# Performance work log

Measured on AMD Instinct MI355X. Metric: run time of the kernel, lower is better.

## Reference

```python
import jax, jax.numpy as jnp
import numpy as np

D = 128
H = 4
DK = D // H


def _spmm(row, col, val, x, n):
    # sparse.mm(adj, x) with adj in COO form: out[row] += val * x[col]
    return jax.ops.segment_sum(val[:, None] * x[col], row, num_segments=n)


def _arrg(h, a1_w, a1_b, a2_w, a2_b):
    return jax.nn.leaky_relu(h @ a1_w + a1_b, negative_slope=0.01) @ a2_w + a2_b


def _cross_attn(x, q_x, q_w, k_w, v_w):
    n, d = x.shape
    m = q_x.shape[0]
    q = (q_x @ q_w).reshape(m, H, DK).transpose(1, 0, 2)   # [H, Q, dk]
    k = (x @ k_w).reshape(n, H, DK).transpose(1, 0, 2)     # [H, N, dk]
    v = (q_x @ v_w).reshape(m, H, DK).transpose(1, 0, 2)   # [H, Q, dk]
    s = jnp.einsum('hnd,hqd->hnq', k, q) / jnp.sqrt(jnp.float32(DK))
    w = jax.nn.softmax(s, axis=-1)                          # softmax over queries
    out = jnp.einsum('hnq,hqd->hnd', w, v).transpose(1, 0, 2).reshape(n, d)
    return out + x


def setup_inputs() -> dict:
    key = jax.random.key(0)
    ks = iter(jax.random.split(key, 64))
    nrm = lambda shape, s=0.05: jax.random.normal(next(ks), shape, jnp.float32) * s
    inp = {}
    inp['trans_w'] = nrm((1, D)); inp['trans_b'] = nrm((D,))
    inp['g_w'] = nrm((D, D));     inp['g_b'] = nrm((D,))
    inp['qg_w'] = nrm((D, D));    inp['qg_b'] = nrm((D,))
    inp['q_w'] = nrm((D, D)); inp['k_w'] = nrm((D, D)); inp['v_w'] = nrm((D, D))
    inp['a1_w'] = nrm((D, 2 * D)); inp['a1_b'] = nrm((2 * D,))
    inp['a2_w'] = nrm((2 * D, D)); inp['a2_b'] = nrm((D,))
    inp['x0'] = jax.random.normal(next(ks), (25000,), jnp.float32)
    inp['q0'] = jax.random.normal(next(ks), (100,), jnp.float32)
    for i in (1, 2, 3):
        inp[f'xin{i}'] = jax.random.normal(next(ks), (25000,), jnp.float32)
        inp[f'qin{i}'] = jax.random.normal(next(ks), (100,), jnp.float32)
    n_sizes = {1: 50000, 2: 75000, 3: 100000}
    q_sizes = {1: 200, 2: 300, 3: 400}
    for i in (1, 2, 3):
        e = 16 * n_sizes[i]
        inp[f'aval{i}'] = jax.random.uniform(next(ks), (e,), jnp.float32)
        inp[f'arow{i}'] = jax.random.randint(next(ks), (e,), 0, n_sizes[i], jnp.int64)
        inp[f'acol{i}'] = jax.random.randint(next(ks), (e,), 0, n_sizes[i], jnp.int64)
        qe = 16 * q_sizes[i]
        inp[f'qval{i}'] = jax.random.uniform(next(ks), (qe,), jnp.float32)
        inp[f'qrow{i}'] = jax.random.randint(next(ks), (qe,), 0, q_sizes[i], jnp.int64)
        inp[f'qcol{i}'] = jax.random.randint(next(ks), (qe,), 0, q_sizes[i], jnp.int64)
    return inp


def reference(trans_w, trans_b, g_w, g_b, qg_w, qg_b, q_w, k_w, v_w,
              a1_w, a1_b, a2_w, a2_b,
              x0, q0, xin1, xin2, xin3, qin1, qin2, qin3,
              aval1, aval2, aval3, qval1, qval2, qval3,
              arow1, acol1, arow2, acol2, arow3, acol3,
              qrow1, qcol1, qrow2, qcol2, qrow3, qcol3):
    trans = lambda v: v[:, None] @ trans_w + trans_b
    x = trans(x0)
    qx = trans(q0)
    steps = [
        (xin1, qin1, arow1, acol1, aval1, qrow1, qcol1, qval1, 50000, 200),
        (xin2, qin2, arow2, acol2, aval2, qrow2, qcol2, qval2, 75000, 300),
        (xin3, qin3, arow3, acol3, aval3, qrow3, qcol3, qval3, 100000, 400),
    ]
    for xin, qin, ar, ac, av, qr, qc, qv, n, m in steps:
        x = jnp.concatenate([x, trans(xin)], axis=0)
        qx = jnp.concatenate([qx, trans(qin)], axis=0)
        x = _spmm(ar, ac, av, x @ g_w + g_b, n)
        qx = _spmm(qr, qc, qv, qx @ qg_w + qg_b, m)
        x = _arrg(x, a1_w, a1_b, a2_w, a2_b)
        qx = _arrg(qx, a1_w, a1_b, a2_w, a2_b)
        x = _cross_attn(x, qx, q_w, k_w, v_w)
    return (x, qx)
```

## Files before the change

### kernel.cpp

```cpp
#include <hip/hip_runtime.h>

typedef unsigned short u16;
typedef __attribute__((ext_vector_type(8))) short bf16x8;
typedef __attribute__((ext_vector_type(4))) float f32x4;
typedef __attribute__((ext_vector_type(2))) unsigned u32x2;

__device__ __forceinline__ float b2f(u16 v) {
    return __uint_as_float(((unsigned)v) << 16);
}
__device__ __forceinline__ u16 f2b(float x) {
    unsigned u = __float_as_uint(x);
    unsigned r = u + 0x7FFFu + ((u >> 16) & 1u);
    return (u16)(r >> 16);
}
__device__ __forceinline__ float4 load_bf4(const u16* p) {
    ushort4 q = *(const ushort4*)p;
    float4 f;
    f.x = b2f(q.x); f.y = b2f(q.y); f.z = b2f(q.z); f.w = b2f(q.w);
    return f;
}
__device__ __forceinline__ float4 in4(const void* p, long off, bool bf) {
    if (bf) return load_bf4((const u16*)p + off);
    return *(const float4*)((const float*)p + off);
}
__device__ __forceinline__ float in1(const void* p, long off, bool bf) {
    if (bf) return b2f(((const u16*)p)[off]);
    return ((const float*)p)[off];
}
__device__ __forceinline__ int inIdx(const void* p, long i, bool i64) {
    return ((const int*)p)[i64 ? 2 * i : i];
}

__global__ void sniff_kernel(const u16* __restrict__ x0bits, const int* __restrict__ arow,
                             int* __restrict__ flags) {
    if (threadIdx.x != 0 || blockIdx.x != 0) return;
    int plaus = 0;
    for (int i = 0; i < 256; ++i) {
        u16 v = x0bits[i];
        int e = (v >> 7) & 0xFF;
        if (v == 0 || (e >= 100 && e <= 135)) plaus++;
    }
    flags[0] = (plaus >= 200) ? 1 : 0;
    int nz = 0;
    for (int i = 1; i < 128; i += 2) nz += (arow[i] != 0);
    flags[1] = (nz == 0) ? 1 : 0;
}

__global__ void trans2_kernel(const void* __restrict__ vx, float* __restrict__ outx, int rowsx,
                              const void* __restrict__ vq, float* __restrict__ outq, int rowsq,
                              const void* __restrict__ tw, const void* __restrict__ tb,
                              const int* __restrict__ flags) {
    const bool bf = flags[0] != 0;
    int t = blockIdx.x * blockDim.x + threadIdx.x;
    int c4 = (t & 31) * 4;
    int r = t >> 5;
    const void* v; float* out;
    if (r < rowsx) { v = vx; out = outx; }
    else { r -= rowsx; if (r >= rowsq) return; v = vq; out = outq; }
    float vv = in1(v, r, bf);
    float4 w4 = in4(tw, c4, bf);
    float4 b4 = in4(tb, c4, bf);
    float4 o;
    o.x = vv * w4.x + b4.x; o.y = vv * w4.y + b4.y;
    o.z = vv * w4.z + b4.z; o.w = vv * w4.w + b4.w;
    *(float4*)(out + (size_t)r * 128 + c4) = o;
}

__global__ void wprep_all_kernel(const void* __restrict__ g_w, const void* __restrict__ qg_w,
                                 const void* __restrict__ a1_w, const void* __restrict__ a2_w,
                                 const void* __restrict__ k_w, const void* __restrict__ q_w,
                                 const void* __restrict__ v_w,
                                 u16* __restrict__ Wg, u16* __restrict__ Wqg,
                                 u16* __restrict__ Wa1, u16* __restrict__ Wa2,
                                 u16* __restrict__ Wk, u16* __restrict__ Wq,
                                 u16* __restrict__ Wv, const int* __restrict__ flags) {
    const bool bf = flags[0] != 0;
    int idx = blockIdx.x * blockDim.x + threadIdx.x;
    const void* src; u16* dst; int K, N, loc;
    if (idx < 32768) {
        if (idx < 16384) { src = g_w; dst = Wg; loc = idx; }
        else { src = qg_w; dst = Wqg; loc = idx - 16384; }
        K = 128; N = 128;
    } else if (idx < 65536) { src = a1_w; dst = Wa1; loc = idx - 32768; K = 128; N = 256; }
    else if (idx < 98304)  { src = a2_w; dst = Wa2; loc = idx - 65536; K = 256; N = 128; }
    else if (idx < 147456) {
        if (idx < 114688) { src = k_w; dst = Wk; loc = idx - 98304; }
        else if (idx < 131072) { src = q_w; dst = Wq; loc = idx - 114688; }
        else { src = v_w; dst = Wv; loc = idx - 131072; }
        K = 128; N = 128;
    } else return;
    int j = loc & 7, lane = (loc >> 3) & 63, t = loc >> 9;
    int KC = K >> 5;
    int kc = t % KC, ct = t / KC;
    int k = kc * 32 + (lane >> 4) * 8 + j;
    int nn = ct * 16 + (lane & 15);
    dst[loc] = f2b(in1(src, (long)k * N + nn, bf));
}

template<int KTOT, int NOUT, bool LEAKY, typename AT, typename CT>
__launch_bounds__(256)
__global__ void gemm_mfma_kernel(const AT* __restrict__ A, const u16* __restrict__ Wf,
                                 const void* __restrict__ bias, CT* __restrict__ C,
                                 int n, const int* __restrict__ flags,
                                 const void* __restrict__ vap, int nprevP,
                                 const void* __restrict__ twp, const void* __restrict__ tbp) {
    constexpr int KC = KTOT / 32;
    constexpr int NT = NOUT / 16;
    __shared__ u16 wlds[KTOT * NOUT];
    {
        const int4* srcw = (const int4*)Wf;
        int4* dstw = (int4*)wlds;
        constexpr int NV = KTOT * NOUT * 2 / 16;
#pragma unroll
        for (int i = 0; i < NV / 256; ++i)
            dstw[i * 256 + threadIdx.x] = srcw[i * 256 + threadIdx.x];
    }
    __syncthreads();
    const bool bf = flags[0] != 0;
    const int lane = threadIdx.x & 63;
    const int wave = threadIdx.x >> 6;
    const int quad = lane >> 4, col = lane & 15;
    const int rbase = (blockIdx.x * 4 + wave) * 16;
    if (rbase >= n) return;
    int node = rbase + col; if (node >= n) node = n - 1;
    f32x4 acc[NT];
#pragma unroll
    for (int ct = 0; ct < NT; ++ct) acc[ct] = (f32x4){0.f, 0.f, 0.f, 0.f};
#pragma unroll
    for (int kc = 0; kc < KC; ++kc) {
        bf16x8 af;
        if constexpr (sizeof(AT) == 2) {
            af = *(const bf16x8*)((const u16*)A + (size_t)node * KTOT + kc * 32 + quad * 8);
        } else {
            int c0 = kc * 32 + quad * 8;
            if (vap && node >= nprevP) {
                float v = in1(vap, node - nprevP, bf);
                float4 w0 = in4(twp, c0, bf), w1 = in4(twp, c0 + 4, bf);
                float4 b0 = in4(tbp, c0, bf), b1 = in4(tbp, c0 + 4, bf);
                af[0] = (short)f2b(v * w0.x + b0.x); af[1] = (short)f2b(v * w0.y + b0.y);
                af[2] = (short)f2b(v * w0.z + b0.z); af[3] = (short)f2b(v * w0.w + b0.w);
                af[4] = (short)f2b(v * w1.x + b1.x); af[5] = (short)f2b(v * w1.y + b1.y);
                af[6] = (short)f2b(v * w1.z + b1.z); af[7] = (short)f2b(v * w1.w + b1.w);
            } else {
                const float* ap = (const float*)A + (size_t)node * KTOT + c0;
                float4 a0 = *(const float4*)ap;
                float4 a1 = *(const float4*)(ap + 4);
                af[0] = (short)f2b(a0.x); af[1] = (short)f2b(a0.y);
                af[2] = (short)f2b(a0.z); af[3] = (short)f2b(a0.w);
                af[4] = (short)f2b(a1.x); af[5] = (short)f2b(a1.y);
                af[6] = (short)f2b(a1.z); af[7] = (short)f2b(a1.w);
            }
        }
#pragma unroll
        for (int ct = 0; ct < NT; ++ct) {
            bf16x8 wf = *(const bf16x8*)(wlds + (((ct * KC + kc) * 64 + lane) * 8));
            acc[ct] = __builtin_amdgcn_mfma_f32_16x16x32_bf16(af, wf, acc[ct], 0, 0, 0);
        }
    }
#pragma unroll
    for (int ct = 0; ct < NT; ++ct) {
        int colg = ct * 16 + col;
        float b = bias ? in1(bias, colg, bf) : 0.f;
#pragma unroll
        for (int r = 0; r < 4; ++r) {
            int row = rbase + quad * 4 + r;
            if (row >= n) continue;
            float v = acc[ct][r] + b;
            if (LEAKY) v = v > 0.f ? v : 0.01f * v;
            if constexpr (sizeof(CT) == 2) C[(size_t)row * NOUT + colg] = (CT)f2b(v);
            else                           C[(size_t)row * NOUT + colg] = (CT)v;
        }
    }
}

__launch_bounds__(256)
__global__ void gemm_qv_kernel(const float* __restrict__ A, const u16* __restrict__ Wfq,
                               const u16* __restrict__ Wfv, u16* __restrict__ Qf,
                               u16* __restrict__ Vf, int m, int mt32) {
    __shared__ u16 wldsq[128 * 128];
    __shared__ u16 wldsv[128 * 128];
    {
        const int4* sq = (const int4*)Wfq;
        const int4* sv = (const int4*)Wfv;
        int4* dq = (int4*)wldsq;
        int4* dv = (int4*)wldsv;
#pragma unroll
        for (int i = 0; i < 8; ++i) {
            dq[i * 256 + threadIdx.x] = sq[i * 256 + threadIdx.x];
            dv[i * 256 + threadIdx.x] = sv[i * 256 + threadIdx.x];
        }
    }
    __syncthreads();
    const int mpad = mt32 * 32;
    const int mt16 = mt32 * 2;
    const int lane = threadIdx.x & 63;
    const int wave = threadIdx.x >> 6;
    const int quad = lane >> 4, col = lane & 15;
    const int rbase = (blockIdx.x * 4 + wave) * 16;
    if (rbase >= mpad) return;
    int node = rbase + col; if (node >= m) node = m - 1;
    f32x4 accq[8], accv[8];
#pragma unroll
    for (int ct = 0; ct < 8; ++ct) {
        accq[ct] = (f32x4){0.f, 0.f, 0.f, 0.f};
        accv[ct] = (f32x4){0.f, 0.f, 0.f, 0.f};
    }
#pragma unroll
    for (int kc = 0; kc < 4; ++kc) {
        const float* ap = A + (size_t)node * 128 + kc * 32 + quad * 8;
        float4 a0 = *(const float4*)ap;
        float4 a1 = *(const float4*)(ap + 4);
        bf16x8 af;
        af[0] = (short)f2b(a0.x); af[1] = (short)f2b(a0.y);
        af[2] = (short)f2b(a0.z); af[3] = (short)f2b(a0.w);
        af[4] = (short)f2b(a1.x); af[5] = (short)f2b(a1.y);
        af[6] = (short)f2b(a1.z); af[7] = (short)f2b(a1.w);
#pragma unroll
        for (int ct = 0; ct < 8; ++ct) {
            bf16x8 wq = *(const bf16x8*)(wldsq + (((ct * 4 + kc) * 64 + lane) * 8));
            bf16x8 wv = *(const bf16x8*)(wldsv + (((ct * 4 + kc) * 64 + lane) * 8));
            accq[ct] = __builtin_amdgcn_mfma_f32_16x16x32_bf16(af, wq, accq[ct], 0, 0, 0);
            accv[ct] = __builtin_amdgcn_mfma_f32_16x16x32_bf16(af, wv, accv[ct], 0, 0, 0);
        }
    }
    const float qscale = 0.17677669529663687f * 1.44269504088896340736f;
#pragma unroll
    for (int ct = 0; ct < 8; ++ct) {
        int colg = ct * 16 + col;
        int h = colg >> 5, dim = colg & 31;
#pragma unroll
        for (int r = 0; r < 4; ++r) {
            int row = rbase + quad * 4 + r;
            if (row >= mpad) continue;
            bool pad = row >= m;
            float vq = pad ? 0.f : accq[ct][r] * qscale;
            float vv = pad ? 0.f : accv[ct][r];
            {
                size_t idx = ((((size_t)h * mt16 + (row >> 4)) * 64)
                              + ((dim >> 3) << 4) + (row & 15)) * 8 + (dim & 7);
                Qf[idx] = f2b(vq);
            }
            {
                size_t idx = (((((size_t)h * mt32 + (row >> 5)) * 2 + (dim >> 4)) * 64)
                              + (((row >> 3) & 3) << 4) + (dim & 15)) * 8 + (row & 7);
                Vf[idx] = f2b(vv);
            }
        }
    }
}

#define RSH 8
#define NBC_MAX 512
#define EPB 4096
#define BSTRIDE 6144

__global__ void ginit_kernel(int* __restrict__ p, int nbc) {
    int i = blockIdx.x * blockDim.x + threadIdx.x;
    if (i < nbc) p[i] = i * BSTRIDE;
}

__launch_bounds__(256)
__global__ void qbuild_kernel(const void* __restrict__ rows, const void* __restrict__ colsin,
                              const void* __restrict__ valsin, int e, int nrows,
                              int2* __restrict__ pack1, int* __restrict__ rowptr,
                              int* __restrict__ rowend, const int* __restrict__ flags) {
    __shared__ int hist[512], cur[512], sc[512];
    const bool bf = flags[0] != 0;
    const bool i64 = flags[1] != 0;
    const int tid = threadIdx.x;
    for (int i = tid; i < 512; i += 256) hist[i] = 0;
    __syncthreads();
    for (int i = tid; i < e; i += 256)
        atomicAdd(&hist[inIdx(rows, i, i64)], 1);
    __syncthreads();
    int v0 = hist[tid], v1 = hist[tid + 256];
    sc[tid] = v0; sc[tid + 256] = v1;
    __syncthreads();
    for (int off = 1; off < 512; off <<= 1) {
        int a = (tid >= off) ? sc[tid - off] : 0;
        int b = sc[tid + 256 - off];
        __syncthreads();
        sc[tid] += a;
        sc[tid + 256] += b;
        __syncthreads();
    }
    {
        int x = sc[tid] - v0;
        cur[tid] = x;
        if (tid < nrows) { rowptr[tid] = x; rowend[tid] = x + v0; }
        int x1 = sc[tid + 256] - v1;
        cur[tid + 256] = x1;
        if (tid + 256 < nrows) { rowptr[tid + 256] = x1; rowend[tid + 256] = x1 + v1; }
    }
    __syncthreads();
    for (int i = tid; i < e; i += 256) {
        int r = inIdx(rows, i, i64);
        int p = atomicAdd(&cur[r], 1);
        pack1[p] = (int2){inIdx(colsin, i, i64), __float_as_int(in1(valsin, i, bf))};
    }
}

__launch_bounds__(256)
__global__ void psort_kernel(const void* __restrict__ rows, const void* __restrict__ colsin,
                             const void* __restrict__ valsin, int e,
                             int* __restrict__ gcur, int2* __restrict__ pack0,
                             int nbc, const int* __restrict__ flags) {
    __shared__ int hist[NBC_MAX];
    __shared__ int scan[NBC_MAX];
    __shared__ int base[NBC_MAX];
    __shared__ int cur[NBC_MAX];
    __shared__ int2 stage[EPB];
    __shared__ u16 binof[EPB];
    const bool bf = flags[0] != 0;
    const bool i64 = flags[1] != 0;
    const int tid = threadIdx.x;
    const long s0 = (long)blockIdx.x * EPB;
    int cnt_e = e - (int)s0; if (cnt_e > EPB) cnt_e = EPB;

    for (int i = tid; i < NBC_MAX; i += 256) hist[i] = 0;
    __syncthreads();
    for (int j = tid; j < cnt_e; j += 256)
        atomicAdd(&hist[inIdx(rows, s0 + j, i64) >> RSH], 1);
    __syncthreads();
    for (int i = tid; i < NBC_MAX; i += 256) scan[i] = hist[i];
    __syncthreads();
    for (int off = 1; off < NBC_MAX; off <<= 1) {
        int a = (tid >= off) ? scan[tid - off] : 0;
        int c = scan[tid + 256 - off];
        __syncthreads();
        scan[tid] += a;
        scan[tid + 256] += c;
        __syncthreads();
    }
    for (int i = tid; i < nbc; i += 256) {
        int h = hist[i];
        cur[i] = scan[i] - h;
        base[i] = h ? atomicAdd(&gcur[i], h) : 0;
    }
    __syncthreads();
    for (int j = tid; j < cnt_e; j += 256) {
        int r = inIdx(rows, s0 + j, i64);
        int bin = r >> RSH;
        int p = atomicAdd(&cur[bin], 1);
        int2 pk;
        pk.x = ((r & ((1 << RSH) - 1)) << 20) | inIdx(colsin, s0 + j, i64);
        pk.y = __float_as_int(in1(valsin, s0 + j, bf));
        stage[p] = pk;
        binof[p] = (u16)bin;
    }
    __syncthreads();
    for (int j = tid; j < cnt_e; j += 256) {
        int bin = binof[j];
        int st = scan[bin] - hist[bin];
        pack0[base[bin] + (j - st)] = stage[j];
    }
}

__launch_bounds__(256)
__global__ void breorder256_kernel(const int2* __restrict__ pack0, int* __restrict__ bend,
                                   int2* __restrict__ pack1,
                                   int* __restrict__ rowptr, int* __restrict__ rowend, int n) {
    __shared__ int hist[256], scan[256], cur[256];
    const int b = blockIdx.x;
    const int s = b * BSTRIDE, e = bend[b];
    const int tid = threadIdx.x;
    hist[tid] = 0;
    __syncthreads();
    if (tid == 0) bend[b] = b * BSTRIDE;
    for (int i = s + tid; i < e; i += 256)
        atomicAdd(&hist[(unsigned)pack0[i].x >> 20], 1);
    __syncthreads();
    scan[tid] = hist[tid];
    __syncthreads();
    for (int off = 1; off < 256; off <<= 1) {
        int a = (tid >= off) ? scan[tid - off] : 0;
        __syncthreads();
        scan[tid] += a;
        __syncthreads();
    }
    int st = s + scan[tid] - hist[tid];
    cur[tid] = st;
    int rg = (b << RSH) + tid;
    if (rg < n) { rowptr[rg] = st; rowend[rg] = st + hist[tid]; }
    __syncthreads();
    for (int i = s + tid; i < e; i += 256) {
        int2 pk = pack0[i];
        int rl = (unsigned)pk.x >> 20;
        int p = atomicAdd(&cur[rl], 1);
        pack1[p] = (int2){pk.x & 0xFFFFF, pk.y};
    }
}

__device__ __forceinline__ void bffma8(float v, uint4 h, float* a) {
    a[0] += v * __uint_as_float(h.x << 16);
    a[1] += v * __uint_as_float(h.x & 0xFFFF0000u);
    a[2] += v * __uint_as_float(h.y << 16);
    a[3] += v * __uint_as_float(h.y & 0xFFFF0000u);
    a[4] += v * __uint_as_float(h.z << 16);
    a[5] += v * __uint_as_float(h.z & 0xFFFF0000u);
    a[6] += v * __uint_as_float(h.w << 16);
    a[7] += v * __uint_as_float(h.w & 0xFFFF0000u);
}
__global__ void spmm_kernel(const u16* __restrict__ H, const int* __restrict__ rowptr,
                            const int* __restrict__ rowend, const int2* __restrict__ pack,
                            u16* __restrict__ out, int n) {
    int w = threadIdx.x >> 6;
    int lane = threadIdx.x & 63;
    int r = blockIdx.x * 4 + w;
    if (r >= n) return;
    const int s16 = lane >> 4;
    const int l16 = lane & 15;
    int s = rowptr[r], e = rowend[r];
    float a[8] = {0.f, 0.f, 0.f, 0.f, 0.f, 0.f, 0.f, 0.f};
    int i = s + s16;
    for (; i + 12 < e; i += 16) {
        int2 p0 = pack[i], p1 = pack[i + 4], p2 = pack[i + 8], p3 = pack[i + 12];
        uint4 h0 = *(const uint4*)(H + (size_t)p0.x * 128 + l16 * 8);
        uint4 h1 = *(const uint4*)(H + (size_t)p1.x * 128 + l16 * 8);
        uint4 h2 = *(const uint4*)(H + (size_t)p2.x * 128 + l16 * 8);
        uint4 h3 = *(const uint4*)(H + (size_t)p3.x * 128 + l16 * 8);
        bffma8(__int_as_float(p0.y), h0, a);
        bffma8(__int_as_float(p1.y), h1, a);
        bffma8(__int_as_float(p2.y), h2, a);
        bffma8(__int_as_float(p3.y), h3, a);
    }
    for (; i < e; i += 4) {
        int2 p0 = pack[i];
        uint4 h0 = *(const uint4*)(H + (size_t)p0.x * 128 + l16 * 8);
        bffma8(__int_as_float(p0.y), h0, a);
    }
#pragma unroll
    for (int k = 0; k < 8; ++k) {
        a[k] += __shfl_xor(a[k], 16, 64);
        a[k] += __shfl_xor(a[k], 32, 64);
    }
    if (s16 == 0) {
        uint4 o;
        o.x = (unsigned)f2b(a[0]) | ((unsigned)f2b(a[1]) << 16);
        o.y = (unsigned)f2b(a[2]) | ((unsigned)f2b(a[3]) << 16);
        o.z = (unsigned)f2b(a[4]) | ((unsigned)f2b(a[5]) << 16);
        o.w = (unsigned)f2b(a[6]) | ((unsigned)f2b(a[7]) << 16);
        *(uint4*)(out + (size_t)r * 128 + l16 * 8) = o;
    }
}

__launch_bounds__(256)
__global__ void attn_mfma_kernel(const u16* __restrict__ Kb, const u16* __restrict__ Qf,
                                 const u16* __restrict__ Vf, float* __restrict__ X,
                                 int n, int m, int mt32, int pad) {
    __shared__ __align__(128) u16 Pbuf_all[4 * 1024];
    const int h = blockIdx.y;
    const int wave = threadIdx.x >> 6;
    const int lane = threadIdx.x & 63;
    const int nb = (blockIdx.x * 4 + wave) * 32;
    if (nb >= n) return;
    const int quad = lane >> 4, col = lane & 15;
    int node0 = nb + col;      if (node0 >= n) node0 = n - 1;
    int node1 = nb + 16 + col; if (node1 >= n) node1 = n - 1;
    bf16x8 kf0 = *(const bf16x8*)(Kb + (size_t)node0 * 128 + h * 32 + quad * 8);
    bf16x8 kf1 = *(const bf16x8*)(Kb + (size_t)node1 * 128 + h * 32 + quad * 8);
    f32x4 O00 = {0.f, 0.f, 0.f, 0.f}, O01 = {0.f, 0.f, 0.f, 0.f};
    f32x4 O10 = {0.f, 0.f, 0.f, 0.f}, O11 = {0.f, 0.f, 0.f, 0.f};
    const f32x4 zero = {0.f, 0.f, 0.f, 0.f};
    float Lp0[4] = {0.f, 0.f, 0.f, 0.f};
    float Lp1[4] = {0.f, 0.f, 0.f, 0.f};
    u16* Pw0 = Pbuf_all + wave * 1024;
    u16* Pw1 = Pw0 + 512;
    uint2* pw0[2]; uint2* pw1[2];
    pw0[0] = (uint2*)(Pw0 + col * 16 + quad * 4);
    pw0[1] = (uint2*)(Pw0 + 256 + col * 16 + quad * 4);
    pw1[0] = (uint2*)(Pw1 + col * 16 + quad * 4);
    pw1[1] = (uint2*)(Pw1 + 256 + col * 16 + quad * 4);
    const unsigned paddr0 = (unsigned)(uintptr_t)Pw0 + (unsigned)(quad * 256 + col * 8);
    const unsigned paddr1 = (unsigned)(uintptr_t)Pw1 + (unsigned)(quad * 256 + col * 8);
    const u16* Qbase = Qf + (size_t)h * (mt32 * 2) * 512;
    const u16* Vbase = Vf + (size_t)h * mt32 * 1024;
    for (int qc = 0; qc < mt32; ++qc) {
#pragma unroll
        for (int half = 0; half < 2; ++half) {
            bf16x8 qfr = *(const bf16x8*)(Qbase + (size_t)(qc * 2 + half) * 512 + lane * 8);
            f32x4 S0 = __builtin_amdgcn_mfma_f32_16x16x32_bf16(kf0, qfr, zero, 0, 0, 0);
            f32x4 S1 = __builtin_amdgcn_mfma_f32_16x16x32_bf16(kf1, qfr, zero, 0, 0, 0);
            float a0 = __builtin_amdgcn_exp2f(fminf(S0[0], 115.f));
            float a1 = __builtin_amdgcn_exp2f(fminf(S0[1], 115.f));
            float a2 = __builtin_amdgcn_exp2f(fminf(S0[2], 115.f));
            float a3 = __builtin_amdgcn_exp2f(fminf(S0[3], 115.f));
            float b0 = __builtin_amdgcn_exp2f(fminf(S1[0], 115.f));
            float b1 = __builtin_amdgcn_exp2f(fminf(S1[1], 115.f));
            float b2 = __builtin_amdgcn_exp2f(fminf(S1[2], 115.f));
            float b3 = __builtin_amdgcn_exp2f(fminf(S1[3], 115.f));
            Lp0[0] += a0; Lp0[1] += a1; Lp0[2] += a2; Lp0[3] += a3;
            Lp1[0] += b0; Lp1[1] += b1; Lp1[2] += b2; Lp1[3] += b3;
            unsigned ra, rb, rc, rd;
            asm volatile("v_cvt_pk_bf16_f32 %0, %1, %2" : "=v"(ra) : "v"(a0), "v"(a1));
            asm volatile("v_cvt_pk_bf16_f32 %0, %1, %2" : "=v"(rb) : "v"(a2), "v"(a3));
            asm volatile("v_cvt_pk_bf16_f32 %0, %1, %2" : "=v"(rc) : "v"(b0), "v"(b1));
            asm volatile("v_cvt_pk_bf16_f32 %0, %1, %2" : "=v"(rd) : "v"(b2), "v"(b3));
            uint2 pka; pka.x = ra; pka.y = rb;
            uint2 pkb; pkb.x = rc; pkb.y = rd;
            *pw0[half] = pka;
            *pw1[half] = pkb;
        }
        asm volatile("s_waitcnt lgkmcnt(0)" ::: "memory");
        u32x2 t0a, t0b, t1a, t1b;
        asm volatile("ds_read_b64_tr_b16 %0, %1" : "=&v"(t0a) : "v"(paddr0) : "memory");
        asm volatile("ds_read_b64_tr_b16 %0, %1 offset:128" : "=&v"(t0b) : "v"(paddr0) : "memory");
        asm volatile("ds_read_b64_tr_b16 %0, %1" : "=&v"(t1a) : "v"(paddr1) : "memory");
        asm volatile("ds_read_b64_tr_b16 %0, %1 offset:128" : "=&v"(t1b) : "v"(paddr1) : "memory");
        asm volatile("s_waitcnt lgkmcnt(0)" ::: "memory");
        __builtin_amdgcn_sched_barrier(0);
        bf16x8 pf0, pf1;
        ((u32x2*)&pf0)[0] = t0a; ((u32x2*)&pf0)[1] = t0b;
        ((u32x2*)&pf1)[0] = t1a; ((u32x2*)&pf1)[1] = t1b;
        bf16x8 v0 = *(const bf16x8*)(Vbase + (size_t)(qc * 2 + 0) * 512 + lane * 8);
        bf16x8 v1 = *(const bf16x8*)(Vbase + (size_t)(qc * 2 + 1) * 512 + lane * 8);
        __builtin_amdgcn_s_setprio(1);
        O00 = __builtin_amdgcn_mfma_f32_16x16x32_bf16(pf0, v0, O00, 0, 0, 0);
        O01 = __builtin_amdgcn_mfma_f32_16x16x32_bf16(pf0, v1, O01, 0, 0, 0);
        O10 = __builtin_amdgcn_mfma_f32_16x16x32_bf16(pf1, v0, O10, 0, 0, 0);
        O11 = __builtin_amdgcn_mfma_f32_16x16x32_bf16(pf1, v1, O11, 0, 0, 0);
        __builtin_amdgcn_s_setprio(0);
    }
#pragma unroll
    for (int mask = 1; mask < 16; mask <<= 1) {
#pragma unroll
        for (int r = 0; r < 4; ++r) {
            Lp0[r] += __shfl_xor(Lp0[r], mask, 64);
            Lp1[r] += __shfl_xor(Lp1[r], mask, 64);
        }
    }
#pragma unroll
    for (int r = 0; r < 4; ++r) {
        int nd = nb + quad * 4 + r;
        if (nd < n) {
            float inv = 1.f / fmaxf(Lp0[r] - (float)pad, 1e-35f);
            float* xp = X + (size_t)nd * 128 + h * 32;
            xp[col]      += O00[r] * inv;
            xp[16 + col] += O01[r] * inv;
        }
        int nd1 = nb + 16 + quad * 4 + r;
        if (nd1 < n) {
            float inv = 1.f / fmaxf(Lp1[r] - (float)pad, 1e-35f);
            float* xp = X + (size_t)nd1 * 128 + h * 32;
            xp[col]      += O10[r] * inv;
            xp[16 + col] += O11[r] * inv;
        }
    }
}

__global__ void out_writer_kernel(const float* __restrict__ X, const float* __restrict__ QX,
                                  void* __restrict__ out, const int* __restrict__ flags) {
    const bool bf = flags[0] != 0;
    const int n4x = 100000 * 128 / 4;
    const int n4t = n4x + 400 * 128 / 4;
    int i = blockIdx.x * blockDim.x + threadIdx.x;
    if (i >= n4t) return;
    float4 v = (i < n4x) ? ((const float4*)X)[i] : ((const float4*)QX)[i - n4x];
    if (bf) {
        ushort4 q; q.x = f2b(v.x); q.y = f2b(v.y); q.z = f2b(v.z); q.w = f2b(v.w);
        ((ushort4*)out)[i] = q;
    } else {
        ((float4*)out)[i] = v;
    }
}

extern "C" void kernel_launch(void* const* d_in, const int* in_sizes, int n_in,
                              void* d_out, int out_size, void* d_ws, size_t ws_size,
                              hipStream_t stream) {
    (void)n_in; (void)out_size; (void)ws_size;
    const void* trans_w = d_in[0];
    const void* trans_b = d_in[1];
    const void* g_w  = d_in[2];
    const void* g_b  = d_in[3];
    const void* qg_w = d_in[4];
    const void* qg_b = d_in[5];
    const void* q_w  = d_in[6];
    const void* k_w  = d_in[7];
    const void* v_w  = d_in[8];
    const void* a1_w = d_in[9];
    const void* a1_b = d_in[10];
    const void* a2_w = d_in[11];
    const void* a2_b = d_in[12];
    const void* x0   = d_in[13];
    const void* q0   = d_in[14];

    int ixin[3], iqin[3], iaval[3], iarow[3], iacol[3], iqval[3], iqrow[3], iqcol[3];
    if (in_sizes[16] == 100) {
        for (int s = 0; s < 3; ++s) {
            ixin[s] = 15 + 2 * s; iqin[s] = 16 + 2 * s;
            int b = 21 + 6 * s;
            iaval[s] = b; iarow[s] = b + 1; iacol[s] = b + 2;
            iqval[s] = b + 3; iqrow[s] = b + 4; iqcol[s] = b + 5;
        }
    } else {
        int xs[3] = {15,16,17}, qs_[3] = {18,19,20};
        int av[3] = {21,22,23}, qv[3] = {24,25,26};
        int ar[3] = {27,29,31}, ac[3] = {28,30,32};
        int qr[3] = {33,35,37}, qc[3] = {34,36,38};
        for (int s = 0; s < 3; ++s) {
            ixin[s]=xs[s]; iqin[s]=qs_[s]; iaval[s]=av[s]; iqval[s]=qv[s];
            iarow[s]=ar[s]; iacol[s]=ac[s]; iqrow[s]=qr[s]; iqcol[s]=qc[s];
        }
    }

    char* p = (char*)d_ws;
    auto alloc = [&](size_t bytes) -> char* {
        char* r = p;
        p += (bytes + 255) & ~(size_t)255;
        return r;
    };
    int*   flags = (int*)alloc(256);
    const int NMAX = 100000;
    const int NBINS = (NMAX + 255) >> RSH;
    float* X   = (float*)alloc((size_t)NMAX * 128 * 4);
    u16*   T1b = (u16*)  alloc((size_t)NMAX * 128 * 2);
    u16*   Xs  = (u16*)  alloc((size_t)NMAX * 128 * 2);
    u16*   T2  = (u16*)  alloc((size_t)NMAX * 256 * 2);
    float* QX  = (float*)alloc((size_t)400 * 128 * 4);
    u16*   QT1b= (u16*)  alloc((size_t)400 * 128 * 2);
    u16*   QXs = (u16*)  alloc((size_t)400 * 128 * 2);
    u16*   QT2 = (u16*)  alloc((size_t)400 * 256 * 2);
    u16*   Qfrag = (u16*)alloc((size_t)4 * 13 * 1024 * 2);
    u16*   Vfrag = (u16*)alloc((size_t)4 * 13 * 1024 * 2);
    u16* Wg  = (u16*)alloc((size_t)128 * 128 * 2);
    u16* Wqg = (u16*)alloc((size_t)128 * 128 * 2);
    u16* Wa1 = (u16*)alloc((size_t)128 * 256 * 2);
    u16* Wa2 = (u16*)alloc((size_t)256 * 128 * 2);
    u16* Wk  = (u16*)alloc((size_t)128 * 128 * 2);
    u16* Wq  = (u16*)alloc((size_t)128 * 128 * 2);
    u16* Wv  = (u16*)alloc((size_t)128 * 128 * 2);
    int2*  csr_pack = (int2*)alloc((size_t)(NBINS + 1) * BSTRIDE * 8);
    int*   bktcur = (int*)alloc((size_t)NBC_MAX * 4);
    int*   rowptr = (int*)alloc((size_t)NMAX * 4);
    int*   rowend = (int*)alloc((size_t)NMAX * 4);
    int2*  pack0  = (int2*)T2;

    sniff_kernel<<<1, 64, 0, stream>>>((const u16*)x0, (const int*)d_in[iarow[0]], flags);

    wprep_all_kernel<<<(147456 + 255) / 256, 256, 0, stream>>>(
        g_w, qg_w, a1_w, a2_w, k_w, q_w, v_w,
        Wg, Wqg, Wa1, Wa2, Wk, Wq, Wv, flags);

    int nprev = in_sizes[13];
    int mprev = in_sizes[14];
    {
        int tot = (nprev + mprev) * 32;
        trans2_kernel<<<(tot + 255) / 256, 256, 0, stream>>>(x0, X, nprev, q0, QX, mprev,
                                                             trans_w, trans_b, flags);
    }
    ginit_kernel<<<(NBC_MAX + 255) / 256, 256, 0, stream>>>(bktcur, NBC_MAX);

    const int ns[3] = {50000, 75000, 100000};
    const int ms[3] = {200, 300, 400};
    for (int s = 0; s < 3; ++s) {
        const int n = ns[s], m = ms[s];
        const int e  = in_sizes[iaval[s]];
        const int qe = in_sizes[iqval[s]];
        const int gb  = (n + 63) / 64;
        const int gqb = (m + 63) / 64;
        const int mt32 = (m + 31) / 32;
        const int pad = mt32 * 32 - m;
        gemm_mfma_kernel<128, 128, false, float, u16><<<gb, 256, 0, stream>>>(
            X, Wg, g_b, T1b, n, flags, d_in[ixin[s]], nprev, trans_w, trans_b);
        {
            int nbc = (n + 255) >> RSH;
            psort_kernel<<<(e + EPB - 1) / EPB, 256, 0, stream>>>(
                d_in[iarow[s]], d_in[iacol[s]], d_in[iaval[s]], e, bktcur, pack0, nbc, flags);
            breorder256_kernel<<<nbc, 256, 0, stream>>>(pack0, bktcur, csr_pack,
                                                        rowptr, rowend, n);
            spmm_kernel<<<(n + 3) / 4, 256, 0, stream>>>(T1b, rowptr, rowend, csr_pack,
                                                         Xs, n);
        }
        gemm_mfma_kernel<128, 128, false, float, u16><<<gqb, 256, 0, stream>>>(
            QX, Wqg, qg_b, QT1b, m, flags, d_in[iqin[s]], mprev, trans_w, trans_b);
        qbuild_kernel<<<1, 256, 0, stream>>>(d_in[iqrow[s]], d_in[iqcol[s]], d_in[iqval[s]],
                                             qe, m, csr_pack, rowptr, rowend, flags);
        spmm_kernel<<<(m + 3) / 4, 256, 0, stream>>>(QT1b, rowptr, rowend, csr_pack,
                                                     QXs, m);
        gemm_mfma_kernel<128, 256, true, u16, u16><<<gb, 256, 0, stream>>>(
            Xs, Wa1, a1_b, T2, n, flags, nullptr, 0, nullptr, nullptr);
        gemm_mfma_kernel<256, 128, false, u16, float><<<gb, 256, 0, stream>>>(
            T2, Wa2, a2_b, X, n, flags, nullptr, 0, nullptr, nullptr);
        gemm_mfma_kernel<128, 256, true, u16, u16><<<gqb, 256, 0, stream>>>(
            QXs, Wa1, a1_b, QT2, m, flags, nullptr, 0, nullptr, nullptr);
        gemm_mfma_kernel<256, 128, false, u16, float><<<gqb, 256, 0, stream>>>(
            QT2, Wa2, a2_b, QX, m, flags, nullptr, 0, nullptr, nullptr);
        gemm_mfma_kernel<128, 128, false, float, u16><<<gb, 256, 0, stream>>>(
            X, Wk, nullptr, T1b, n, flags, nullptr, 0, nullptr, nullptr);
        gemm_qv_kernel<<<(mt32 * 32 + 63) / 64, 256, 0, stream>>>(QX, Wq, Wv, Qfrag, Vfrag, m, mt32);
        attn_mfma_kernel<<<dim3((n + 127) / 128, 4), 256, 0, stream>>>(
            T1b, Qfrag, Vfrag, X, n, m, mt32, pad);
        nprev = n;
        mprev = m;
    }

    const int n4t = (100000 + 400) * 128 / 4;
    out_writer_kernel<<<(n4t + 255) / 256, 256, 0, stream>>>(X, QX, d_out, flags);
}
```

Measured before the change: 1.126 ms.

## Fuse second MLP GEMM with K and Q/V projections via LDS staging

The second arrg GEMM (256->128) is merged with the following K projection for nodes, and with the Q/V projection for queries. Each 16-row tile's bf16 result is staged in LDS and fed straight into the next MFMA GEMM. This removes two kernel launches and the round trip where X was written in fp32 and re-read for the K GEMM. The cost is a large LDS footprint (weights plus staging tiles, about 128KB for the node kernel), which limits occupancy.

```diff
diff --git a/kernel.cpp b/kernel.cpp
--- a/kernel.cpp
+++ b/kernel.cpp
@@ -173,32 +173,135 @@
     }
 }
 
+__launch_bounds__(512)
+__global__ void mlp2k_kernel(const u16* __restrict__ A, const u16* __restrict__ Wf2,
+                             const u16* __restrict__ Wfk, const void* __restrict__ a2b,
+                             float* __restrict__ X, u16* __restrict__ Kb,
+                             int n, const int* __restrict__ flags) {
+    __shared__ u16 wlds2[256 * 128];
+    __shared__ u16 wldsk[128 * 128];
+    __shared__ __align__(16) u16 xt[8][16 * 136];
+    const int tid = threadIdx.x;
+    {
+        const int4* s2 = (const int4*)Wf2;
+        int4* d2 = (int4*)wlds2;
+        for (int i = tid; i < 4096; i += 512) d2[i] = s2[i];
+        const int4* sk = (const int4*)Wfk;
+        int4* dk = (int4*)wldsk;
+        for (int i = tid; i < 2048; i += 512) dk[i] = sk[i];
+    }
+    __syncthreads();
+    const bool bf = flags[0] != 0;
+    const int lane = tid & 63;
+    const int wave = tid >> 6;
+    const int quad = lane >> 4, col = lane & 15;
+    const int rbase = (blockIdx.x * 8 + wave) * 16;
+    int node = rbase + col; if (node >= n) node = n - 1;
+    f32x4 acc[8];
+#pragma unroll
+    for (int ct = 0; ct < 8; ++ct) acc[ct] = (f32x4){0.f, 0.f, 0.f, 0.f};
+#pragma unroll
+    for (int kc = 0; kc < 8; ++kc) {
+        bf16x8 af = *(const bf16x8*)(A + (size_t)node * 256 + kc * 32 + quad * 8);
+#pragma unroll
+        for (int ct = 0; ct < 8; ++ct) {
+            bf16x8 wf = *(const bf16x8*)(wlds2 + (((ct * 8 + kc) * 64 + lane) * 8));
+            acc[ct] = __builtin_amdgcn_mfma_f32_16x16x32_bf16(af, wf, acc[ct], 0, 0, 0);
+        }
+    }
+    u16* xw = xt[wave];
+#pragma unroll
+    for (int ct = 0; ct < 8; ++ct) {
+        int colg = ct * 16 + col;
+        float b = in1(a2b, colg, bf);
+#pragma unroll
+        for (int r = 0; r < 4; ++r) {
+            int row = rbase + quad * 4 + r;
+            float v = acc[ct][r] + b;
+            if (row < n) X[(size_t)row * 128 + colg] = v;
+            xw[(quad * 4 + r) * 136 + colg] = f2b(v);
+        }
+    }
+    __syncthreads();
+    f32x4 akk[8];
+#pragma unroll
+    for (int ct = 0; ct < 8; ++ct) akk[ct] = (f32x4){0.f, 0.f, 0.f, 0.f};
+#pragma unroll
+    for (int kc = 0; kc < 4; ++kc) {
+        bf16x8 af = *(const bf16x8*)(xw + col * 136 + kc * 32 + quad * 8);
+#pragma unroll
+        for (int ct = 0; ct < 8; ++ct) {
+            bf16x8 wf = *(const bf16x8*)(wldsk + (((ct * 4 + kc) * 64 + lane) * 8));
+            akk[ct] = __builtin_amdgcn_mfma_f32_16x16x32_bf16(af, wf, akk[ct], 0, 0, 0);
+        }
+    }
+#pragma unroll
+    for (int ct = 0; ct < 8; ++ct) {
+        int colg = ct * 16 + col;
+#pragma unroll
+        for (int r = 0; r < 4; ++r) {
+            int row = rbase + quad * 4 + r;
+            if (row < n) Kb[(size_t)row * 128 + colg] = f2b(akk[ct][r]);
+        }
+    }
+}
+
 __launch_bounds__(256)
-__global__ void gemm_qv_kernel(const float* __restrict__ A, const u16* __restrict__ Wfq,
-                               const u16* __restrict__ Wfv, u16* __restrict__ Qf,
-                               u16* __restrict__ Vf, int m, int mt32) {
+__global__ void mlp2qv_kernel(const u16* __restrict__ A, const u16* __restrict__ Wf2,
+                              const u16* __restrict__ Wfq, const u16* __restrict__ Wfv,
+                              const void* __restrict__ a2b, float* __restrict__ QX,
+                              u16* __restrict__ Qf, u16* __restrict__ Vf,
+                              int m, int mt32, const int* __restrict__ flags) {
+    __shared__ u16 wlds2[256 * 128];
     __shared__ u16 wldsq[128 * 128];
     __shared__ u16 wldsv[128 * 128];
+    __shared__ __align__(16) u16 xt[4][16 * 136];
+    const int tid = threadIdx.x;
     {
+        const int4* s2 = (const int4*)Wf2;
+        int4* d2 = (int4*)wlds2;
+        for (int i = tid; i < 4096; i += 256) d2[i] = s2[i];
         const int4* sq = (const int4*)Wfq;
         const int4* sv = (const int4*)Wfv;
         int4* dq = (int4*)wldsq;
         int4* dv = (int4*)wldsv;
-#pragma unroll
-        for (int i = 0; i < 8; ++i) {
-            dq[i * 256 + threadIdx.x] = sq[i * 256 + threadIdx.x];
-            dv[i * 256 + threadIdx.x] = sv[i * 256 + threadIdx.x];
-        }
-    }
-    __syncthreads();
+        for (int i = tid; i < 2048; i += 256) { dq[i] = sq[i]; dv[i] = sv[i]; }
+    }
+    __syncthreads();
+    const bool bf = flags[0] != 0;
     const int mpad = mt32 * 32;
     const int mt16 = mt32 * 2;
-    const int lane = threadIdx.x & 63;
-    const int wave = threadIdx.x >> 6;
+    const int lane = tid & 63;
+    const int wave = tid >> 6;
     const int quad = lane >> 4, col = lane & 15;
     const int rbase = (blockIdx.x * 4 + wave) * 16;
-    if (rbase >= mpad) return;
     int node = rbase + col; if (node >= m) node = m - 1;
+    f32x4 acc[8];
+#pragma unroll
+    for (int ct = 0; ct < 8; ++ct) acc[ct] = (f32x4){0.f, 0.f, 0.f, 0.f};
+#pragma unroll
+    for (int kc = 0; kc < 8; ++kc) {
+        bf16x8 af = *(const bf16x8*)(A + (size_t)node * 256 + kc * 32 + quad * 8);
+#pragma unroll
+        for (int ct = 0; ct < 8; ++ct) {
+            bf16x8 wf = *(const bf16x8*)(wlds2 + (((ct * 8 + kc) * 64 + lane) * 8));
+            acc[ct] = __builtin_amdgcn_mfma_f32_16x16x32_bf16(af, wf, acc[ct], 0, 0, 0);
+        }
+    }
+    u16* xw = xt[wave];
+#pragma unroll
+    for (int ct = 0; ct < 8; ++ct) {
+        int colg = ct * 16 + col;
+        float b = in1(a2b, colg, bf);
+#pragma unroll
+        for (int r = 0; r < 4; ++r) {
+            int row = rbase + quad * 4 + r;
+            float v = acc[ct][r] + b;
+            if (row < m) QX[(size_t)row * 128 + colg] = v;
+            xw[(quad * 4 + r) * 136 + colg] = f2b(v);
+        }
+    }
+    __syncthreads();
     f32x4 accq[8], accv[8];
 #pragma unroll
     for (int ct = 0; ct < 8; ++ct) {
@@ -207,14 +310,7 @@
     }
 #pragma unroll
     for (int kc = 0; kc < 4; ++kc) {
-        const float* ap = A + (size_t)node * 128 + kc * 32 + quad * 8;
-        float4 a0 = *(const float4*)ap;
-        float4 a1 = *(const float4*)(ap + 4);
-        bf16x8 af;
-        af[0] = (short)f2b(a0.x); af[1] = (short)f2b(a0.y);
-        af[2] = (short)f2b(a0.z); af[3] = (short)f2b(a0.w);
-        af[4] = (short)f2b(a1.x); af[5] = (short)f2b(a1.y);
-        af[6] = (short)f2b(a1.z); af[7] = (short)f2b(a1.w);
+        bf16x8 af = *(const bf16x8*)(xw + col * 136 + kc * 32 + quad * 8);
 #pragma unroll
         for (int ct = 0; ct < 8; ++ct) {
             bf16x8 wq = *(const bf16x8*)(wldsq + (((ct * 4 + kc) * 64 + lane) * 8));
@@ -679,15 +775,12 @@
                                                      QXs, m);
         gemm_mfma_kernel<128, 256, true, u16, u16><<<gb, 256, 0, stream>>>(
             Xs, Wa1, a1_b, T2, n, flags, nullptr, 0, nullptr, nullptr);
-        gemm_mfma_kernel<256, 128, false, u16, float><<<gb, 256, 0, stream>>>(
-            T2, Wa2, a2_b, X, n, flags, nullptr, 0, nullptr, nullptr);
         gemm_mfma_kernel<128, 256, true, u16, u16><<<gqb, 256, 0, stream>>>(
             QXs, Wa1, a1_b, QT2, m, flags, nullptr, 0, nullptr, nullptr);
-        gemm_mfma_kernel<256, 128, false, u16, float><<<gqb, 256, 0, stream>>>(
-            QT2, Wa2, a2_b, QX, m, flags, nullptr, 0, nullptr, nullptr);
-        gemm_mfma_kernel<128, 128, false, float, u16><<<gb, 256, 0, stream>>>(
-            X, Wk, nullptr, T1b, n, flags, nullptr, 0, nullptr, nullptr);
-        gemm_qv_kernel<<<(mt32 * 32 + 63) / 64, 256, 0, stream>>>(QX, Wq, Wv, Qfrag, Vfrag, m, mt32);
+        mlp2k_kernel<<<(n + 127) / 128, 512, 0, stream>>>(T2, Wa2, Wk, a2_b, X, T1b,
+                                                          n, flags);
+        mlp2qv_kernel<<<(mt32 * 32 + 63) / 64, 256, 0, stream>>>(
+            QT2, Wa2, Wq, Wv, a2_b, QX, Qfrag, Vfrag, m, mt32, flags);
         attn_mfma_kernel<<<dim3((n + 127) / 128, 4), 256, 0, stream>>>(
             T1b, Qfrag, Vfrag, X, n, m, mt32, pad);
         nprev = n;
```

Measured after the change: 1.071 ms. 4.8% less time.
